# Kernel tuning notes

Measured on AMD Instinct MI355X. Metric: run time of the kernel, lower is better.

## Reference

```python
import jax, jax.numpy as jnp
import numpy as np

EPS = 1e-6

def _det3(m):
    return (m[..., 0, 0] * m[..., 1, 1] * m[..., 2, 2]
            + m[..., 0, 1] * m[..., 1, 2] * m[..., 2, 0]
            + m[..., 1, 0] * m[..., 2, 1] * m[..., 0, 2]
            - m[..., 2, 0] * m[..., 1, 1] * m[..., 0, 2]
            - m[..., 0, 0] * m[..., 2, 1] * m[..., 1, 2]
            - m[..., 1, 0] * m[..., 0, 1] * m[..., 2, 2])

def _inv3(m):
    a, b, c = m[..., 0, 0], m[..., 0, 1], m[..., 0, 2]
    d, e, f = m[..., 1, 0], m[..., 1, 1], m[..., 1, 2]
    g, h, i = m[..., 2, 0], m[..., 2, 1], m[..., 2, 2]
    adj = jnp.stack([
        jnp.stack([e * i - f * h, c * h - b * i, b * f - c * e], -1),
        jnp.stack([f * g - d * i, a * i - c * g, c * d - a * f], -1),
        jnp.stack([d * h - e * g, b * g - a * h, a * e - b * d], -1)], -2)
    return adj / _det3(m)[..., None, None]

def setup_inputs() -> dict:
    key = jax.random.key(0)
    ks = jax.random.split(key, 12)
    N, B, DH = 100000, 2048, 256
    idx = jnp.sort(jnp.concatenate([jnp.arange(B, dtype=jnp.int32),
                                    jax.random.randint(ks[0], (N - B,), 0, B, dtype=jnp.int32)]))
    return {
        "t": jax.random.uniform(ks[1], (B, 1), jnp.float32, 0.01, 0.99),
        "h": jax.random.normal(ks[2], (N, DH), jnp.float32),
        "pos": jax.random.normal(ks[3], (N, 3), jnp.float32),
        "eps_h": jax.random.normal(ks[4], (N, DH), jnp.float32),
        "eps_pos": jax.random.normal(ks[5], (N, 3), jnp.float32),
        "gparam_h": jax.random.normal(ks[6], (1, 1), jnp.float32),
        "gparam_pos": jax.random.normal(ks[7], (1, 1), jnp.float32),
        "W_mu": jax.random.normal(ks[8], (DH, DH), jnp.float32) / np.sqrt(DH),
        "W_r1": jax.random.normal(ks[9], (DH, 2 * DH), jnp.float32) / np.sqrt(DH),
        "W_r2": jax.random.normal(ks[10], (2 * DH, DH), jnp.float32) / np.sqrt(2 * DH),
        "index": idx,
        "num_graphs": B,
    }


def _forward(t, h, pos, eps_h, eps_pos, gparam_h, gparam_pos, W_mu, W_r1, W_r2, index, B):
    eye = jnp.eye(3, dtype=h.dtype)
    seg_sum = lambda x: jax.ops.segment_sum(x, index, num_segments=B)
    counts = seg_sum(jnp.ones((index.shape[0],), h.dtype))  # [B]

    def scatter_center(x):  # x - per-graph mean, gathered back
        mean = seg_sum(x) / counts[:, None]
        return x - mean[index]

    # volatility g(t): per-graph, gathered to nodes
    g_h = (0.1 + jax.nn.softplus(gparam_h) * t)[index]      # [N,1]
    g_pos = (0.1 + jax.nn.softplus(gparam_pos) * t)[index]  # [N,1]

    def f_net(t_, hh, pp):  # surrogate forward transformation f
        tn = t_[index]                                      # [N,1]
        mu_h = (hh @ W_mu) * (1.0 - tn)
        sigma_h = 0.1 + 0.9 * tn                            # [N,1]
        mu_pos = pp * (1.0 - tn)
        nrm = pp / (jnp.linalg.norm(pp, axis=-1, keepdims=True) + EPS)
        a = (0.2 + 0.8 * tn)[..., None]                     # [N,1,1]
        b = (0.1 * tn)[..., None]
        U = a * eye + b * (nrm[:, :, None] * nrm[:, None, :])  # [N,3,3]
        return mu_h, sigma_h, mu_pos, U

    def z_pos_fn(mu, U, eps):
        return mu + scatter_center(jnp.einsum('nij,nj->ni', U, eps))

    def score_pos_fn(eps, U, inv_U=None, C=None):
        if inv_U is None or C is None:
            inv_U = _inv3(U)
            inv_V = _inv3(seg_sum(inv_U))
            C = inv_V[index] @ (inv_U - eye)
        y = jnp.einsum('nji,nj->ni', inv_U, eps)
        ybar = seg_sum(y)
        c = jnp.einsum('nji,nj->ni', C, ybar[index])
        return scatter_center(c - y)  # zero_cog_score=True

    def solve_pos_fn(U, prel):
        inv_U = _inv3(U)
        inv_V = _inv3(seg_sum(inv_U))
        C = inv_V[index] @ (inv_U - eye)
        c = seg_sum(jnp.einsum('nij,nj->ni', C, prel))[index]
        eps = jnp.einsum('nij,nj->ni', inv_U, prel - c)
        return eps, inv_U, C

    bdrift = lambda dz, score, g: dz - 0.5 * g ** 2 * score

    # ---- target backward drift (time_derivative via jvp over t) ----
    (mu_h, sig_h, mu_p, U), (dmu_h, dsig_h, dmu_p, dU) = jax.jvp(
        lambda tt: f_net(tt, h, pos), (t,), (jnp.ones_like(t),))
    z_h = mu_h + sig_h * eps_h
    dz_h = dmu_h + dsig_h * eps_h
    z_p = z_pos_fn(mu_p, U, eps_pos)
    dz_p = z_pos_fn(dmu_p, dU, eps_pos)
    tgt_h = bdrift(dz_h, -eps_h / sig_h, g_h)
    tgt_p = bdrift(dz_p, score_pos_fn(eps_pos, U), g_pos)

    # ---- approximate backward drift ('x0' parameterization) ----
    h_r = jnp.tanh(z_h @ W_r1) @ W_r2   # reconstructor r
    pos_r = z_p * 0.9
    (mu_h2, sig_h2, mu_p2, U2), (dmu_h2, dsig_h2, dmu_p2, dU2) = jax.jvp(
        lambda tt: f_net(tt, h_r, pos_r), (t,), (jnp.ones_like(t),))
    eps_h2 = (z_h - mu_h2) / sig_h2
    eps_p2, inv_U2, C2 = solve_pos_fn(U2, z_p - mu_p2)
    dz_h2 = dmu_h2 + dsig_h2 * eps_h2
    dz_p2 = z_pos_fn(dmu_p2, dU2, eps_p2)
    apx_h = bdrift(dz_h2, -eps_h2 / sig_h2, g_h)
    apx_p = bdrift(dz_p2, score_pos_fn(eps_p2, U2, inv_U2, C2), g_pos)

    # ---- 'simple' loss: mse(approx/g, target/g) ----
    loss_h = jnp.mean(((apx_h - tgt_h) / g_h) ** 2)
    loss_p = jnp.mean(((apx_p - tgt_p) / g_pos) ** 2)
    return loss_h, loss_p


def reference(t, h, pos, eps_h, eps_pos, gparam_h, gparam_pos, W_mu, W_r1, W_r2, index, num_graphs):
    return _forward(t, h, pos, eps_h, eps_pos, gparam_h, gparam_pos, W_mu, W_r1, W_r2, index, num_graphs)
```

## Files before the change

kernel.cpp:

```cpp
#include <hip/hip_runtime.h>
#include <math.h>

#define NTHREADS 256
#define EPSC 1e-6f
#define NPL 3

typedef short bf16x8 __attribute__((ext_vector_type(8)));
typedef float f32x4  __attribute__((ext_vector_type(4)));

#define GLDS(srcp, dstp) __builtin_amdgcn_global_load_lds( \
    (const __attribute__((address_space(1))) void*)(srcp), \
    (__attribute__((address_space(3))) void*)(dstp), 16, 0, 0)

__device__ __forceinline__ ushort f2bf(float x) {
  union { float f; unsigned u; } v; v.f = x;
  unsigned r = v.u + 0x7FFFu + ((v.u >> 16) & 1u);
  return (ushort)(r >> 16);
}
__device__ __forceinline__ float bf2f(ushort x) {
  union { unsigned u; float f; } v; v.u = ((unsigned)x) << 16;
  return v.f;
}
__device__ __forceinline__ float tanh_fast(float x) {
  float xc = fminf(fmaxf(x, -15.f), 15.f);
  float e = __expf(2.f * xc);
  return (e - 1.f) / (e + 1.f);
}

__device__ __forceinline__ void inv3x3(const float m[9], float o[9]) {
  float a=m[0],b=m[1],c=m[2],d=m[3],e=m[4],f=m[5],g=m[6],h=m[7],i=m[8];
  float det = a*e*i + b*f*g + d*h*c - g*e*c - a*h*f - d*b*i;
  float r = 1.0f/det;
  o[0]=(e*i-f*h)*r; o[1]=(c*h-b*i)*r; o[2]=(b*f-c*e)*r;
  o[3]=(f*g-d*i)*r; o[4]=(a*i-c*g)*r; o[5]=(c*d-a*f)*r;
  o[6]=(d*h-e*g)*r; o[7]=(b*g-a*h)*r; o[8]=(a*e-b*d)*r;
}

__device__ __forceinline__ float wred(float v) {
#pragma unroll
  for (int o = 32; o > 0; o >>= 1) v += __shfl_xor(v, o, 64);
  return v;
}

__global__ __launch_bounds__(64) void pos_fused(
    int N, const float* __restrict__ pos, const float* __restrict__ epsp,
    const int* __restrict__ index, const float* __restrict__ t,
    const float* __restrict__ gpp, double* __restrict__ lossp)
{
  const int b = blockIdx.x;
  const int lane = threadIdx.x;

  int lo = 0, hi = N;
  while (lo < hi) { int mid = (lo + hi) >> 1; if (index[mid] < b) lo = mid + 1; else hi = mid; }
  const int start = lo;
  hi = N;
  while (lo < hi) { int mid = (lo + hi) >> 1; if (index[mid] < b + 1) lo = mid + 1; else hi = mid; }
  const int end = lo;
  const int cnt = end - start;
  const float fn = (float)cnt, rc = 1.0f / fn;

  const float tn  = t[b];
  const float a1  = 0.2f + 0.8f*tn, b1 = 0.1f*tn;
  const float omt = 1.0f - tn;
  const float sp  = log1pf(expf(gpp[0]));
  const float gp  = 0.1f + sp*tn;
  const float hg  = 0.5f*gp*gp;
  const float rgp = 1.0f/gp;
  const float pscale = 1.0f - 0.9f*omt;

  float iU[NPL][9], yv[NPL][3], wv[NPL][3], dwv[NPL][3], pv[NPL][3];
  float Vs[9] = {0}, wb[3] = {0}, dwb[3] = {0}, yb[3] = {0};
#pragma unroll
  for (int k = 0; k < NPL; ++k) {
    const int n = start + k*64 + lane;
    if (n < end) {
      const float px = pos[3*(size_t)n+0], py = pos[3*(size_t)n+1], pz = pos[3*(size_t)n+2];
      const float ex = epsp[3*(size_t)n+0], ey = epsp[3*(size_t)n+1], ez = epsp[3*(size_t)n+2];
      pv[k][0]=px; pv[k][1]=py; pv[k][2]=pz;
      const float pn = sqrtf(px*px+py*py+pz*pz) + EPSC;
      const float nx = px/pn, ny = py/pn, nz = pz/pn;
      const float nd = nx*ex + ny*ey + nz*ez;
      wv[k][0]=a1*ex + b1*nd*nx; wv[k][1]=a1*ey + b1*nd*ny; wv[k][2]=a1*ez + b1*nd*nz;
      dwv[k][0]=0.8f*ex + 0.1f*nd*nx; dwv[k][1]=0.8f*ey + 0.1f*nd*ny; dwv[k][2]=0.8f*ez + 0.1f*nd*nz;
      const float U[9] = { a1 + b1*nx*nx, b1*nx*ny,      b1*nx*nz,
                           b1*ny*nx,      a1 + b1*ny*ny, b1*ny*nz,
                           b1*nz*nx,      b1*nz*ny,      a1 + b1*nz*nz };
      inv3x3(U, iU[k]);
      yv[k][0] = iU[k][0]*ex + iU[k][3]*ey + iU[k][6]*ez;
      yv[k][1] = iU[k][1]*ex + iU[k][4]*ey + iU[k][7]*ez;
      yv[k][2] = iU[k][2]*ex + iU[k][5]*ey + iU[k][8]*ez;
#pragma unroll
      for (int j = 0; j < 9; ++j) Vs[j] += iU[k][j];
#pragma unroll
      for (int j = 0; j < 3; ++j) { wb[j]+=wv[k][j]; dwb[j]+=dwv[k][j]; yb[j]+=yv[k][j]; }
    }
  }
#pragma unroll
  for (int j = 0; j < 9; ++j) Vs[j] = wred(Vs[j]);
#pragma unroll
  for (int j = 0; j < 3; ++j) { wb[j]=wred(wb[j]); dwb[j]=wred(dwb[j]); yb[j]=wred(yb[j]); }

  float iV[9]; inv3x3(Vs, iV);
  float wm[3], dwm[3], u1[3], s1m[3];
#pragma unroll
  for (int i = 0; i < 3; ++i) { wm[i] = wb[i]*rc; dwm[i] = dwb[i]*rc; }
#pragma unroll
  for (int i = 0; i < 3; ++i) u1[i] = iV[0*3+i]*yb[0] + iV[1*3+i]*yb[1] + iV[2*3+i]*yb[2];
#pragma unroll
  for (int i = 0; i < 3; ++i) {
    const float csy = Vs[0*3+i]*u1[0] + Vs[1*3+i]*u1[1] + Vs[2*3+i]*u1[2] - fn*u1[i];
    s1m[i] = (csy - yb[i]) * rc;
  }

  float tg[NPL][3], zp[NPL][3], iU2[NPL][9], qv[NPL][3];
  float Vs2[9] = {0}, qs[3] = {0}, ps[3] = {0};
#pragma unroll
  for (int k = 0; k < NPL; ++k) {
    const int n = start + k*64 + lane;
    if (n < end) {
#pragma unroll
      for (int i = 0; i < 3; ++i) {
        const float c1 = iU[k][0*3+i]*u1[0] + iU[k][1*3+i]*u1[1] + iU[k][2*3+i]*u1[2] - u1[i];
        const float score1 = c1 - yv[k][i] - s1m[i];
        tg[k][i] = -pv[k][i] + dwv[k][i] - dwm[i] - hg*score1;
        zp[k][i] = pv[k][i]*omt + wv[k][i] - wm[i];
      }
      const float rx = 0.9f*zp[k][0], ry = 0.9f*zp[k][1], rz = 0.9f*zp[k][2];
      const float rn = sqrtf(rx*rx+ry*ry+rz*rz) + EPSC;
      const float nx = rx/rn, ny = ry/rn, nz = rz/rn;
      const float U2[9] = { a1 + b1*nx*nx, b1*nx*ny,      b1*nx*nz,
                            b1*ny*nx,      a1 + b1*ny*ny, b1*ny*nz,
                            b1*nz*nx,      b1*nz*ny,      a1 + b1*nz*nz };
      inv3x3(U2, iU2[k]);
      float prel[3];
#pragma unroll
      for (int i = 0; i < 3; ++i) prel[i] = zp[k][i]*pscale;
#pragma unroll
      for (int i = 0; i < 3; ++i)
        qv[k][i] = iU2[k][i*3+0]*prel[0] + iU2[k][i*3+1]*prel[1] + iU2[k][i*3+2]*prel[2];
#pragma unroll
      for (int j = 0; j < 9; ++j) Vs2[j] += iU2[k][j];
#pragma unroll
      for (int j = 0; j < 3; ++j) { qs[j] += qv[k][j]; ps[j] += prel[j]; }
    }
  }
#pragma unroll
  for (int j = 0; j < 9; ++j) Vs2[j] = wred(Vs2[j]);
#pragma unroll
  for (int j = 0; j < 3; ++j) { qs[j] = wred(qs[j]); ps[j] = wred(ps[j]); }

  float iV2[9]; inv3x3(Vs2, iV2);
  float cb2[3];
#pragma unroll
  for (int i = 0; i < 3; ++i)
    cb2[i] = iV2[i*3+0]*(qs[0]-ps[0]) + iV2[i*3+1]*(qs[1]-ps[1]) + iV2[i*3+2]*(qs[2]-ps[2]);

  float y2v[NPL][3], dw2v[NPL][3];
  float yb2[3] = {0}, dwb2[3] = {0};
#pragma unroll
  for (int k = 0; k < NPL; ++k) {
    const int n = start + k*64 + lane;
    if (n < end) {
      float e[3];
#pragma unroll
      for (int i = 0; i < 3; ++i)
        e[i] = qv[k][i] - (iU2[k][i*3+0]*cb2[0] + iU2[k][i*3+1]*cb2[1] + iU2[k][i*3+2]*cb2[2]);
#pragma unroll
      for (int i = 0; i < 3; ++i)
        y2v[k][i] = iU2[k][0*3+i]*e[0] + iU2[k][1*3+i]*e[1] + iU2[k][2*3+i]*e[2];
      const float rx = 0.9f*zp[k][0], ry = 0.9f*zp[k][1], rz = 0.9f*zp[k][2];
      const float rn = sqrtf(rx*rx+ry*ry+rz*rz) + EPSC;
      const float nx = rx/rn, ny = ry/rn, nz = rz/rn;
      const float nd = nx*e[0] + ny*e[1] + nz*e[2];
      dw2v[k][0] = 0.8f*e[0] + 0.1f*nd*nx;
      dw2v[k][1] = 0.8f*e[1] + 0.1f*nd*ny;
      dw2v[k][2] = 0.8f*e[2] + 0.1f*nd*nz;
#pragma unroll
      for (int j = 0; j < 3; ++j) { yb2[j] += y2v[k][j]; dwb2[j] += dw2v[k][j]; }
    }
  }
#pragma unroll
  for (int j = 0; j < 3; ++j) { yb2[j] = wred(yb2[j]); dwb2[j] = wred(dwb2[j]); }

  float u2[3], s2m[3], dw2m[3];
#pragma unroll
  for (int i = 0; i < 3; ++i) u2[i] = iV2[0*3+i]*yb2[0] + iV2[1*3+i]*yb2[1] + iV2[2*3+i]*yb2[2];
#pragma unroll
  for (int i = 0; i < 3; ++i) {
    const float csy = Vs2[0*3+i]*u2[0] + Vs2[1*3+i]*u2[1] + Vs2[2*3+i]*u2[2] - fn*u2[i];
    s2m[i] = (csy - yb2[i]) * rc;
    dw2m[i] = dwb2[i] * rc;
  }

  float acc = 0.0f;
#pragma unroll
  for (int k = 0; k < NPL; ++k) {
    const int n = start + k*64 + lane;
    if (n < end) {
#pragma unroll
      for (int i = 0; i < 3; ++i) {
        const float c2 = iU2[k][0*3+i]*u2[0] + iU2[k][1*3+i]*u2[1] + iU2[k][2*3+i]*u2[2] - u2[i];
        const float score2 = c2 - y2v[k][i] - s2m[i];
        const float dz2 = -0.9f*zp[k][i] + dw2v[k][i] - dw2m[i];
        const float apx = dz2 - hg*score2;
        const float d = (apx - tg[k][i]) * rgp;
        acc += d*d;
      }
    }
  }
  acc = wred(acc);
  if (lane == 0) atomicAdd(lossp, (double)acc);
}

__global__ __launch_bounds__(NTHREADS) void cvt_bf16(
    const float4* __restrict__ in, ushort4* __restrict__ out, int n4)
{
  for (int i = blockIdx.x*blockDim.x + threadIdx.x; i < n4; i += gridDim.x*blockDim.x) {
    float4 v = in[i];
    out[i] = make_ushort4(f2bf(v.x), f2bf(v.y), f2bf(v.z), f2bf(v.w));
  }
}

__global__ __launch_bounds__(NTHREADS) void transpose_cvt(
    const float* __restrict__ in, ushort* __restrict__ out, int K, int Nn)
{
  __shared__ float ts[32][33];
  const int tx = threadIdx.x & 31, ty = threadIdx.x >> 5;
  const int nb = blockIdx.x*32, kb = blockIdx.y*32;
#pragma unroll
  for (int r = 0; r < 4; ++r)
    ts[ty + r*8][tx] = in[(size_t)(kb + ty + r*8)*Nn + nb + tx];
  __syncthreads();
#pragma unroll
  for (int r = 0; r < 4; ++r)
    out[(size_t)(nb + ty + r*8)*K + kb + tx] = f2bf(ts[tx][ty + r*8]);
}

__global__ __launch_bounds__(256) void gemm_wcomb(
    const ushort* __restrict__ A, const ushort* __restrict__ Bt,
    int K, int Nn, int Mvalid, ushort* __restrict__ OutB)
{
  __shared__ __align__(16) ushort As[128*32];
  __shared__ __align__(16) ushort Bs[128*32];
  const int tid = threadIdx.x;
  const int row0 = blockIdx.y*128, col0 = blockIdx.x*128;
  const int wave = tid >> 6, lane = tid & 63;
  const int wm = (wave & 1)*64, wn = (wave >> 1)*64;
  const int lm = lane & 15, lq = lane >> 4;

  f32x4 acc[4][4];
#pragma unroll
  for (int i = 0; i < 4; ++i)
#pragma unroll
    for (int j = 0; j < 4; ++j) { acc[i][j][0]=0.f; acc[i][j][1]=0.f; acc[i][j][2]=0.f; acc[i][j][3]=0.f; }

  const int c0 = tid, c1 = tid + 256;
  const int r0a = c0 >> 2, k0a = (c0 & 3) << 3;
  const int r1a = c1 >> 2, k1a = (c1 & 3) << 3;

  for (int k0 = 0; k0 < K; k0 += 32) {
    __syncthreads();
    GLDS(A  + (size_t)(row0 + r0a)*K + k0 + k0a, As + c0*8);
    GLDS(A  + (size_t)(row0 + r1a)*K + k0 + k1a, As + c1*8);
    GLDS(Bt + (size_t)(col0 + r0a)*K + k0 + k0a, Bs + c0*8);
    GLDS(Bt + (size_t)(col0 + r1a)*K + k0 + k1a, Bs + c1*8);
    __syncthreads();

    bf16x8 af[4], bfr[4];
#pragma unroll
    for (int i = 0; i < 4; ++i)
      af[i] = *(const bf16x8*)&As[(wm + i*16 + lm)*32 + lq*8];
#pragma unroll
    for (int j = 0; j < 4; ++j)
      bfr[j] = *(const bf16x8*)&Bs[(wn + j*16 + lm)*32 + lq*8];
#pragma unroll
    for (int i = 0; i < 4; ++i)
#pragma unroll
      for (int j = 0; j < 4; ++j)
        acc[i][j] = __builtin_amdgcn_mfma_f32_16x16x32_bf16(af[i], bfr[j], acc[i][j], 0, 0, 0);
  }

#pragma unroll
  for (int i = 0; i < 4; ++i) {
#pragma unroll
    for (int reg = 0; reg < 4; ++reg) {
      const int r = row0 + wm + i*16 + lq*4 + reg;
#pragma unroll
      for (int j = 0; j < 4; ++j) {
        const int cc = col0 + wn + j*16 + lm;
        OutB[(size_t)cc*Mvalid + r] = f2bf(acc[i][j][reg]);
      }
    }
  }
}

__global__ __launch_bounds__(256, 2) void fused_h(
    const ushort* __restrict__ hb, const ushort* __restrict__ wmut,
    const ushort* __restrict__ wr1t, const ushort* __restrict__ wct,
    const float* __restrict__ eps, const int* __restrict__ index,
    const float* __restrict__ t, const float* __restrict__ gph,
    int N, double* __restrict__ lossAcc)
{
  __shared__ __align__(16) ushort zs[64*256];
  __shared__ __align__(16) ushort t1s[64*128];
  __shared__ __align__(16) ushort bstg[4*4096];

  const int tid = threadIdx.x;
  const int row0 = blockIdx.x * 64;
  const int wave = tid >> 6, lane = tid & 63;
  const int lm = lane & 15, lq = lane >> 4;
  const int wn  = wave * 64;
  const int wn2 = wave * 32;
  ushort* const bsw = bstg + wave*4096;

  bf16x8 af[8][4];
#pragma unroll
  for (int k = 0; k < 4; ++k)
#pragma unroll
    for (int i = 0; i < 4; ++i)
      af[k][i] = *(const bf16x8*)(hb + (size_t)(row0 + i*16 + lm)*256 + k*32 + lq*8);

#pragma unroll
  for (int c = 0; c < 4; ++c) {
    const int ch = c*64 + lane;
    GLDS(wmut + (size_t)(wn + (ch>>2))*256 + ((ch&3)<<3), bsw + ch*8);
  }

  f32x4 acc1[4][4];
#pragma unroll
  for (int i = 0; i < 4; ++i)
#pragma unroll
    for (int j = 0; j < 4; ++j) { acc1[i][j][0]=0.f; acc1[i][j][1]=0.f; acc1[i][j][2]=0.f; acc1[i][j][3]=0.f; }

#pragma unroll
  for (int k = 0; k < 8; ++k) {
    if (k < 4) {
#pragma unroll
      for (int i = 0; i < 4; ++i)
        af[k+4][i] = *(const bf16x8*)(hb + (size_t)(row0 + i*16 + lm)*256 + (k+4)*32 + lq*8);
    }
    if (k < 7) {
#pragma unroll
      for (int c = 0; c < 4; ++c) {
        const int ch = c*64 + lane;
        GLDS(wmut + (size_t)(wn + (ch>>2))*256 + (k+1)*32 + ((ch&3)<<3),
             bsw + ((k+1)&1)*2048 + ch*8);
      }
    }
    if (k < 4)      { asm volatile("s_waitcnt vmcnt(8)" ::: "memory"); }
    else if (k < 7) { asm volatile("s_waitcnt vmcnt(4)" ::: "memory"); }
    else            { asm volatile("s_waitcnt vmcnt(0)" ::: "memory"); }
    __builtin_amdgcn_sched_barrier(0);

    const ushort* cb = bsw + (k&1)*2048;
    bf16x8 bfr[4];
#pragma unroll
    for (int j = 0; j < 4; ++j)
      bfr[j] = *(const bf16x8*)&cb[(j*16 + lm)*32 + lq*8];
#pragma unroll
    for (int i = 0; i < 4; ++i)
#pragma unroll
      for (int j = 0; j < 4; ++j)
        acc1[i][j] = __builtin_amdgcn_mfma_f32_16x16x32_bf16(af[k][i], bfr[j], acc1[i][j], 0, 0, 0);
  }

#pragma unroll
  for (int c = 0; c < 2; ++c) {
    const int ch = c*64 + lane;
    GLDS(wr1t + (size_t)(wn2 + (ch>>2))*256 + ((ch&3)<<3), bsw + ch*8);
  }

  unsigned hmp[4][4][2];
#pragma unroll
  for (int i = 0; i < 4; ++i) {
#pragma unroll
    for (int reg = 0; reg < 4; ++reg) {
      const int rb = i*16 + lq*4 + reg;
      const int r = row0 + rb;
      const int rcl = (r < N) ? r : (N - 1);
      const float tn = t[index[rcl]];
      const float s0 = 1.0f - tn, s1 = 0.1f + 0.9f*tn;
#pragma unroll
      for (int j = 0; j < 4; ++j) {
        const int cc = wn + j*16 + lm;
        const float hm = acc1[i][j][reg];
        const unsigned hv = (unsigned)f2bf(hm);
        if (reg & 1) hmp[i][j][reg >> 1] |= hv << 16;
        else         hmp[i][j][reg >> 1]  = hv;
        const float z = hm*s0 + s1*eps[(size_t)rcl*256 + cc];
        zs[rb*256 + (cc ^ ((rb & 7) << 3))] = f2bf(z);
      }
    }
  }
  __syncthreads();

  f32x4 accL[4][4];
#pragma unroll
  for (int i = 0; i < 4; ++i)
#pragma unroll
    for (int j = 0; j < 4; ++j) { accL[i][j][0]=0.f; accL[i][j][1]=0.f; accL[i][j][2]=0.f; accL[i][j][3]=0.f; }

  for (int c2 = 0; c2 < 4; ++c2) {
    f32x4 acct[4][2];
#pragma unroll
    for (int i = 0; i < 4; ++i)
#pragma unroll
      for (int j = 0; j < 2; ++j) { acct[i][j][0]=0.f; acct[i][j][1]=0.f; acct[i][j][2]=0.f; acct[i][j][3]=0.f; }

#pragma unroll
    for (int k = 0; k < 8; ++k) {
      if (k < 7) {
#pragma unroll
        for (int c = 0; c < 2; ++c) {
          const int ch = c*64 + lane;
          GLDS(wr1t + (size_t)(c2*128 + wn2 + (ch>>2))*256 + (k+1)*32 + ((ch&3)<<3),
               bsw + ((k+1)&1)*2048 + ch*8);
        }
        asm volatile("s_waitcnt vmcnt(2)" ::: "memory");
      } else {
        asm volatile("s_waitcnt vmcnt(0)" ::: "memory");
      }
      __builtin_amdgcn_sched_barrier(0);

      const ushort* cb = bsw + (k&1)*2048;
      bf16x8 azf[4], bfr[2];
#pragma unroll
      for (int i = 0; i < 4; ++i) {
        const int r = i*16 + lm;
        const int c = k*32 + lq*8;
        azf[i] = *(const bf16x8*)&zs[r*256 + (c ^ ((r & 7) << 3))];
      }
#pragma unroll
      for (int j = 0; j < 2; ++j)
        bfr[j] = *(const bf16x8*)&cb[(j*16 + lm)*32 + lq*8];
#pragma unroll
      for (int i = 0; i < 4; ++i)
#pragma unroll
        for (int j = 0; j < 2; ++j)
          acct[i][j] = __builtin_amdgcn_mfma_f32_16x16x32_bf16(azf[i], bfr[j], acct[i][j], 0, 0, 0);
    }

#pragma unroll
    for (int c = 0; c < 4; ++c) {
      const int ch = c*64 + lane;
      GLDS(wct + (size_t)(wn + (ch>>2))*512 + c2*128 + ((ch&3)<<3), bsw + ch*8);
    }
    __syncthreads();

#pragma unroll
    for (int i = 0; i < 4; ++i)
#pragma unroll
      for (int j = 0; j < 2; ++j)
#pragma unroll
        for (int reg = 0; reg < 4; ++reg) {
          const int rb = i*16 + lq*4 + reg;
          const int c = wn2 + j*16 + lm;
          t1s[rb*128 + (c ^ ((rb & 7) << 3))] = f2bf(tanh_fast(acct[i][j][reg]));
        }
    __syncthreads();

#pragma unroll
    for (int k = 0; k < 4; ++k) {
      if (k < 3) {
#pragma unroll
        for (int c = 0; c < 4; ++c) {
          const int ch = c*64 + lane;
          GLDS(wct + (size_t)(wn + (ch>>2))*512 + c2*128 + (k+1)*32 + ((ch&3)<<3),
               bsw + ((k+1)&1)*2048 + ch*8);
        }
        asm volatile("s_waitcnt vmcnt(4)" ::: "memory");
      } else {
        asm volatile("s_waitcnt vmcnt(0)" ::: "memory");
      }
      __builtin_amdgcn_sched_barrier(0);

      const ushort* cb = bsw + (k&1)*2048;
      bf16x8 atf[4], bfr[4];
#pragma unroll
      for (int i = 0; i < 4; ++i) {
        const int r = i*16 + lm;
        const int c = k*32 + lq*8;
        atf[i] = *(const bf16x8*)&t1s[r*128 + (c ^ ((r & 7) << 3))];
      }
#pragma unroll
      for (int j = 0; j < 4; ++j)
        bfr[j] = *(const bf16x8*)&cb[(j*16 + lm)*32 + lq*8];
#pragma unroll
      for (int i = 0; i < 4; ++i)
#pragma unroll
        for (int j = 0; j < 4; ++j)
          accL[i][j] = __builtin_amdgcn_mfma_f32_16x16x32_bf16(atf[i], bfr[j], accL[i][j], 0, 0, 0);
    }

    if (c2 < 3) {
#pragma unroll
      for (int c = 0; c < 2; ++c) {
        const int ch = c*64 + lane;
        GLDS(wr1t + (size_t)((c2+1)*128 + wn2 + (ch>>2))*256 + ((ch&3)<<3), bsw + ch*8);
      }
    }
  }

  const float sp = log1pf(expf(gph[0]));
  float local = 0.f;
#pragma unroll
  for (int i = 0; i < 4; ++i) {
#pragma unroll
    for (int reg = 0; reg < 4; ++reg) {
      const int rb = i*16 + lq*4 + reg;
      const int r = row0 + rb;
      if (r < N) {
        const float tn = t[index[r]];
        const float gh  = 0.1f + sp*tn;
        const float sig = 0.1f + 0.9f*tn;
        const float fac = 1.0f + (0.9f + 0.5f*gh*gh/sig)*(1.0f - tn)/sig;
        const float sc  = fac/gh;
#pragma unroll
        for (int j = 0; j < 4; ++j) {
          const unsigned pw = hmp[i][j][reg >> 1];
          const ushort hv = (reg & 1) ? (ushort)(pw >> 16) : (ushort)(pw & 0xffffu);
          const float d = (bf2f(hv) - accL[i][j][reg]) * sc;
          local += d*d;
        }
      }
    }
  }
  double dv = (double)local;
#pragma unroll
  for (int off = 32; off > 0; off >>= 1) dv += __shfl_down(dv, off, 64);
  if (lane == 0) atomicAdd(lossAcc, dv);
}

__global__ void finalize_kernel(const double* lossh, const double* lossp,
                                float* out, int N, int DH)
{
  if (threadIdx.x == 0) {
    out[0] = (float)(lossh[0] / ((double)N * (double)DH));
    out[1] = (float)(lossp[0] / ((double)N * 3.0));
  }
}

extern "C" void kernel_launch(void* const* d_in, const int* in_sizes, int n_in,
                              void* d_out, int out_size, void* d_ws, size_t ws_size,
                              hipStream_t stream) {
  const float* t      = (const float*)d_in[0];
  const float* h      = (const float*)d_in[1];
  const float* pos    = (const float*)d_in[2];
  const float* eps_h  = (const float*)d_in[3];
  const float* eps_p  = (const float*)d_in[4];
  const float* gph    = (const float*)d_in[5];
  const float* gpp    = (const float*)d_in[6];
  const float* W_mu   = (const float*)d_in[7];
  const float* W_r1   = (const float*)d_in[8];
  const float* W_r2   = (const float*)d_in[9];
  const int*   index  = (const int*)d_in[10];
  const int B = in_sizes[0];
  const int N = in_sizes[10];
  const int DH = 256, DH2 = 512;
  const int NPAD = 100352;

  char* ws = (char*)d_ws;
  size_t off = 0;
  auto alloc = [&](size_t nbytes) { size_t o = off; off += (nbytes + 255) & ~(size_t)255; return o; };

  size_t o_loss = alloc(16);
  size_t o_hb   = alloc((size_t)NPAD*DH*2);
  size_t o_wmut = alloc((size_t)DH*DH*2);
  size_t o_wr1t = alloc((size_t)DH2*DH*2);
  size_t o_wr2b = alloc((size_t)DH2*DH*2);
  size_t o_wct  = alloc((size_t)DH*DH2*2);

  hipMemsetAsync(ws + o_loss, 0, 16, stream);

  double* lossh = (double*)(ws + o_loss);
  double* lossp = lossh + 1;
  ushort* hb   = (ushort*)(ws + o_hb);
  ushort* wmut = (ushort*)(ws + o_wmut);
  ushort* wr1t = (ushort*)(ws + o_wr1t);
  ushort* wr2b = (ushort*)(ws + o_wr2b);
  ushort* wct  = (ushort*)(ws + o_wct);

  pos_fused<<<B, 64, 0, stream>>>(N, pos, eps_p, index, t, gpp, lossp);

  cvt_bf16<<<2048, NTHREADS, 0, stream>>>((const float4*)h, (ushort4*)hb, N*DH/4);
  cvt_bf16<<<128, NTHREADS, 0, stream>>>((const float4*)W_r2, (ushort4*)wr2b, DH2*DH/4);
  transpose_cvt<<<dim3(DH/32,  DH/32), NTHREADS, 0, stream>>>(W_mu, wmut, DH, DH);
  transpose_cvt<<<dim3(DH2/32, DH/32), NTHREADS, 0, stream>>>(W_r1, wr1t, DH, DH2);

  gemm_wcomb<<<dim3(DH/128, DH2/128), 256, 0, stream>>>(
      wr2b, wmut, DH, DH, DH2, wct);

  const int mg64 = (N + 63) / 64;
  fused_h<<<mg64, 256, 0, stream>>>(
      hb, wmut, wr1t, wct, eps_h, index, t, gph, N, lossh);

  finalize_kernel<<<1, 64, 0, stream>>>(lossh, lossp, (float*)d_out, N, DH);
}
```

Before: 478.9 us.

## Merge prep kernels, fold pos path into main kernel, drop LDS weight staging

Combines the four conversion/transpose kernels into one multi-role launch and runs the per-graph position loss as extra blocks of the main h kernel, cutting the number of launches. The main kernel now reads weight fragments straight from global memory instead of staging them in LDS with async loads, which frees shared memory so launch bounds can rise to 3 blocks per CU. The combined weight matrix is stored negated so the second GEMM accumulates onto the first GEMM's accumulator, removing the packed hm registers and the subtraction. The risks are uncoalesced, higher-latency direct global weight loads with no explicit prefetch, and the pos blocks now sharing the grid with the GEMM blocks.

Result: slower. 545.5 us (+13.9%).

```diff
diff --git a/kernel.cpp b/kernel.cpp
--- a/kernel.cpp
+++ b/kernel.cpp
@@ -42,14 +42,12 @@
   return v;
 }
 
-__global__ __launch_bounds__(64) void pos_fused(
-    int N, const float* __restrict__ pos, const float* __restrict__ epsp,
+__device__ void pos_graph(
+    int b, int lane, int N,
+    const float* __restrict__ pos, const float* __restrict__ epsp,
     const int* __restrict__ index, const float* __restrict__ t,
     const float* __restrict__ gpp, double* __restrict__ lossp)
 {
-  const int b = blockIdx.x;
-  const int lane = threadIdx.x;
-
   int lo = 0, hi = N;
   while (lo < hi) { int mid = (lo + hi) >> 1; if (index[mid] < b) lo = mid + 1; else hi = mid; }
   const int start = lo;
@@ -212,28 +210,47 @@
   if (lane == 0) atomicAdd(lossp, (double)acc);
 }
 
-__global__ __launch_bounds__(NTHREADS) void cvt_bf16(
-    const float4* __restrict__ in, ushort4* __restrict__ out, int n4)
-{
-  for (int i = blockIdx.x*blockDim.x + threadIdx.x; i < n4; i += gridDim.x*blockDim.x) {
-    float4 v = in[i];
-    out[i] = make_ushort4(f2bf(v.x), f2bf(v.y), f2bf(v.z), f2bf(v.w));
-  }
-}
-
-__global__ __launch_bounds__(NTHREADS) void transpose_cvt(
-    const float* __restrict__ in, ushort* __restrict__ out, int K, int Nn)
+__global__ __launch_bounds__(NTHREADS) void prep_all(
+    const float4* __restrict__ h, ushort4* __restrict__ hb, int n4h,
+    const float4* __restrict__ wr2, ushort4* __restrict__ wr2b, int n4w,
+    const float* __restrict__ wmu, ushort* __restrict__ wmut,
+    const float* __restrict__ wr1, ushort* __restrict__ wr1t)
 {
   __shared__ float ts[32][33];
-  const int tx = threadIdx.x & 31, ty = threadIdx.x >> 5;
-  const int nb = blockIdx.x*32, kb = blockIdx.y*32;
-#pragma unroll
-  for (int r = 0; r < 4; ++r)
-    ts[ty + r*8][tx] = in[(size_t)(kb + ty + r*8)*Nn + nb + tx];
-  __syncthreads();
-#pragma unroll
-  for (int r = 0; r < 4; ++r)
-    out[(size_t)(nb + ty + r*8)*K + kb + tx] = f2bf(ts[tx][ty + r*8]);
+  const int bid = blockIdx.x;
+  if (bid < 2048) {
+    for (int i = bid*NTHREADS + threadIdx.x; i < n4h; i += 2048*NTHREADS) {
+      float4 v = h[i];
+      hb[i] = make_ushort4(f2bf(v.x), f2bf(v.y), f2bf(v.z), f2bf(v.w));
+    }
+  } else if (bid < 2176) {
+    for (int i = (bid-2048)*NTHREADS + threadIdx.x; i < n4w; i += 128*NTHREADS) {
+      float4 v = wr2[i];
+      wr2b[i] = make_ushort4(f2bf(v.x), f2bf(v.y), f2bf(v.z), f2bf(v.w));
+    }
+  } else if (bid < 2240) {
+    const int vb = bid - 2176;
+    const int nb = (vb & 7)*32, kb = (vb >> 3)*32;
+    const int tx = threadIdx.x & 31, ty = threadIdx.x >> 5;
+#pragma unroll
+    for (int r = 0; r < 4; ++r)
+      ts[ty + r*8][tx] = wmu[(size_t)(kb + ty + r*8)*256 + nb + tx];
+    __syncthreads();
+#pragma unroll
+    for (int r = 0; r < 4; ++r)
+      wmut[(size_t)(nb + ty + r*8)*256 + kb + tx] = f2bf(ts[tx][ty + r*8]);
+  } else {
+    const int vb = bid - 2240;
+    const int nb = (vb & 15)*32, kb = (vb >> 4)*32;
+    const int tx = threadIdx.x & 31, ty = threadIdx.x >> 5;
+#pragma unroll
+    for (int r = 0; r < 4; ++r)
+      ts[ty + r*8][tx] = wr1[(size_t)(kb + ty + r*8)*512 + nb + tx];
+    __syncthreads();
+#pragma unroll
+    for (int r = 0; r < 4; ++r)
+      wr1t[(size_t)(nb + ty + r*8)*256 + kb + tx] = f2bf(ts[tx][ty + r*8]);
+  }
 }
 
 __global__ __launch_bounds__(256) void gemm_wcomb(
@@ -288,13 +305,16 @@
 #pragma unroll
       for (int j = 0; j < 4; ++j) {
         const int cc = col0 + wn + j*16 + lm;
-        OutB[(size_t)cc*Mvalid + r] = f2bf(acc[i][j][reg]);
-      }
-    }
-  }
-}
-
-__global__ __launch_bounds__(256, 2) void fused_h(
+        OutB[(size_t)cc*Mvalid + r] = f2bf(-acc[i][j][reg]);
+      }
+    }
+  }
+}
+
+__global__ __launch_bounds__(256, 3) void fused_main(
+    int PB, int Bg,
+    const float* __restrict__ pos, const float* __restrict__ epsp,
+    const float* __restrict__ gpp, double* __restrict__ lossp,
     const ushort* __restrict__ hb, const ushort* __restrict__ wmut,
     const ushort* __restrict__ wr1t, const ushort* __restrict__ wct,
     const float* __restrict__ eps, const int* __restrict__ index,
@@ -303,74 +323,42 @@
 {
   __shared__ __align__(16) ushort zs[64*256];
   __shared__ __align__(16) ushort t1s[64*128];
-  __shared__ __align__(16) ushort bstg[4*4096];
-
-  const int tid = threadIdx.x;
-  const int row0 = blockIdx.x * 64;
-  const int wave = tid >> 6, lane = tid & 63;
+
+  const int wave = threadIdx.x >> 6, lane = threadIdx.x & 63;
+
+  if (blockIdx.x < PB) {
+    const int b = blockIdx.x*4 + wave;
+    if (b < Bg) pos_graph(b, lane, N, pos, epsp, index, t, gpp, lossp);
+    return;
+  }
+
+  const int row0 = (blockIdx.x - PB) * 64;
   const int lm = lane & 15, lq = lane >> 4;
   const int wn  = wave * 64;
   const int wn2 = wave * 32;
-  ushort* const bsw = bstg + wave*4096;
-
-  bf16x8 af[8][4];
-#pragma unroll
-  for (int k = 0; k < 4; ++k)
+
+  f32x4 acc[4][4];
+#pragma unroll
+  for (int i = 0; i < 4; ++i)
+#pragma unroll
+    for (int j = 0; j < 4; ++j) { acc[i][j][0]=0.f; acc[i][j][1]=0.f; acc[i][j][2]=0.f; acc[i][j][3]=0.f; }
+
+#pragma unroll
+  for (int k = 0; k < 8; ++k) {
+    bf16x8 a_[4], b_[4];
 #pragma unroll
     for (int i = 0; i < 4; ++i)
-      af[k][i] = *(const bf16x8*)(hb + (size_t)(row0 + i*16 + lm)*256 + k*32 + lq*8);
-
-#pragma unroll
-  for (int c = 0; c < 4; ++c) {
-    const int ch = c*64 + lane;
-    GLDS(wmut + (size_t)(wn + (ch>>2))*256 + ((ch&3)<<3), bsw + ch*8);
-  }
-
-  f32x4 acc1[4][4];
-#pragma unroll
-  for (int i = 0; i < 4; ++i)
-#pragma unroll
-    for (int j = 0; j < 4; ++j) { acc1[i][j][0]=0.f; acc1[i][j][1]=0.f; acc1[i][j][2]=0.f; acc1[i][j][3]=0.f; }
-
-#pragma unroll
-  for (int k = 0; k < 8; ++k) {
-    if (k < 4) {
-#pragma unroll
-      for (int i = 0; i < 4; ++i)
-        af[k+4][i] = *(const bf16x8*)(hb + (size_t)(row0 + i*16 + lm)*256 + (k+4)*32 + lq*8);
-    }
-    if (k < 7) {
-#pragma unroll
-      for (int c = 0; c < 4; ++c) {
-        const int ch = c*64 + lane;
-        GLDS(wmut + (size_t)(wn + (ch>>2))*256 + (k+1)*32 + ((ch&3)<<3),
-             bsw + ((k+1)&1)*2048 + ch*8);
-      }
-    }
-    if (k < 4)      { asm volatile("s_waitcnt vmcnt(8)" ::: "memory"); }
-    else if (k < 7) { asm volatile("s_waitcnt vmcnt(4)" ::: "memory"); }
-    else            { asm volatile("s_waitcnt vmcnt(0)" ::: "memory"); }
-    __builtin_amdgcn_sched_barrier(0);
-
-    const ushort* cb = bsw + (k&1)*2048;
-    bf16x8 bfr[4];
+      a_[i] = *(const bf16x8*)(hb + (size_t)(row0 + i*16 + lm)*256 + k*32 + lq*8);
 #pragma unroll
     for (int j = 0; j < 4; ++j)
-      bfr[j] = *(const bf16x8*)&cb[(j*16 + lm)*32 + lq*8];
+      b_[j] = *(const bf16x8*)(wmut + (size_t)(wn + j*16 + lm)*256 + k*32 + lq*8);
 #pragma unroll
     for (int i = 0; i < 4; ++i)
 #pragma unroll
       for (int j = 0; j < 4; ++j)
-        acc1[i][j] = __builtin_amdgcn_mfma_f32_16x16x32_bf16(af[k][i], bfr[j], acc1[i][j], 0, 0, 0);
-  }
-
-#pragma unroll
-  for (int c = 0; c < 2; ++c) {
-    const int ch = c*64 + lane;
-    GLDS(wr1t + (size_t)(wn2 + (ch>>2))*256 + ((ch&3)<<3), bsw + ch*8);
-  }
-
-  unsigned hmp[4][4][2];
+        acc[i][j] = __builtin_amdgcn_mfma_f32_16x16x32_bf16(a_[i], b_[j], acc[i][j], 0, 0, 0);
+  }
+
 #pragma unroll
   for (int i = 0; i < 4; ++i) {
 #pragma unroll
@@ -383,22 +371,12 @@
 #pragma unroll
       for (int j = 0; j < 4; ++j) {
         const int cc = wn + j*16 + lm;
-        const float hm = acc1[i][j][reg];
-        const unsigned hv = (unsigned)f2bf(hm);
-        if (reg & 1) hmp[i][j][reg >> 1] |= hv << 16;
-        else         hmp[i][j][reg >> 1]  = hv;
-        const float z = hm*s0 + s1*eps[(size_t)rcl*256 + cc];
+        const float z = acc[i][j][reg]*s0 + s1*eps[(size_t)rcl*256 + cc];
         zs[rb*256 + (cc ^ ((rb & 7) << 3))] = f2bf(z);
       }
     }
   }
   __syncthreads();
-
-  f32x4 accL[4][4];
-#pragma unroll
-  for (int i = 0; i < 4; ++i)
-#pragma unroll
-    for (int j = 0; j < 4; ++j) { accL[i][j][0]=0.f; accL[i][j][1]=0.f; accL[i][j][2]=0.f; accL[i][j][3]=0.f; }
 
   for (int c2 = 0; c2 < 4; ++c2) {
     f32x4 acct[4][2];
@@ -409,44 +387,29 @@
 
 #pragma unroll
     for (int k = 0; k < 8; ++k) {
-      if (k < 7) {
-#pragma unroll
-        for (int c = 0; c < 2; ++c) {
-          const int ch = c*64 + lane;
-          GLDS(wr1t + (size_t)(c2*128 + wn2 + (ch>>2))*256 + (k+1)*32 + ((ch&3)<<3),
-               bsw + ((k+1)&1)*2048 + ch*8);
-        }
-        asm volatile("s_waitcnt vmcnt(2)" ::: "memory");
-      } else {
-        asm volatile("s_waitcnt vmcnt(0)" ::: "memory");
-      }
-      __builtin_amdgcn_sched_barrier(0);
-
-      const ushort* cb = bsw + (k&1)*2048;
-      bf16x8 azf[4], bfr[2];
+      bf16x8 az[4], b_[2];
 #pragma unroll
       for (int i = 0; i < 4; ++i) {
         const int r = i*16 + lm;
         const int c = k*32 + lq*8;
-        azf[i] = *(const bf16x8*)&zs[r*256 + (c ^ ((r & 7) << 3))];
+        az[i] = *(const bf16x8*)&zs[r*256 + (c ^ ((r & 7) << 3))];
       }
 #pragma unroll
       for (int j = 0; j < 2; ++j)
-        bfr[j] = *(const bf16x8*)&cb[(j*16 + lm)*32 + lq*8];
+        b_[j] = *(const bf16x8*)(wr1t + (size_t)(c2*128 + wn2 + j*16 + lm)*256 + k*32 + lq*8);
 #pragma unroll
       for (int i = 0; i < 4; ++i)
 #pragma unroll
         for (int j = 0; j < 2; ++j)
-          acct[i][j] = __builtin_amdgcn_mfma_f32_16x16x32_bf16(azf[i], bfr[j], acct[i][j], 0, 0, 0);
-    }
-
-#pragma unroll
-    for (int c = 0; c < 4; ++c) {
-      const int ch = c*64 + lane;
-      GLDS(wct + (size_t)(wn + (ch>>2))*512 + c2*128 + ((ch&3)<<3), bsw + ch*8);
-    }
+          acct[i][j] = __builtin_amdgcn_mfma_f32_16x16x32_bf16(az[i], b_[j], acct[i][j], 0, 0, 0);
+    }
+
+    bf16x8 pb[4];
+#pragma unroll
+    for (int j = 0; j < 4; ++j)
+      pb[j] = *(const bf16x8*)(wct + (size_t)(wn + j*16 + lm)*512 + c2*128 + lq*8);
+
     __syncthreads();
-
 #pragma unroll
     for (int i = 0; i < 4; ++i)
 #pragma unroll
@@ -461,43 +424,26 @@
 
 #pragma unroll
     for (int k = 0; k < 4; ++k) {
-      if (k < 3) {
-#pragma unroll
-        for (int c = 0; c < 4; ++c) {
-          const int ch = c*64 + lane;
-          GLDS(wct + (size_t)(wn + (ch>>2))*512 + c2*128 + (k+1)*32 + ((ch&3)<<3),
-               bsw + ((k+1)&1)*2048 + ch*8);
-        }
-        asm volatile("s_waitcnt vmcnt(4)" ::: "memory");
-      } else {
-        asm volatile("s_waitcnt vmcnt(0)" ::: "memory");
-      }
-      __builtin_amdgcn_sched_barrier(0);
-
-      const ushort* cb = bsw + (k&1)*2048;
-      bf16x8 atf[4], bfr[4];
+      bf16x8 at[4], b_[4];
 #pragma unroll
       for (int i = 0; i < 4; ++i) {
         const int r = i*16 + lm;
         const int c = k*32 + lq*8;
-        atf[i] = *(const bf16x8*)&t1s[r*128 + (c ^ ((r & 7) << 3))];
-      }
-#pragma unroll
-      for (int j = 0; j < 4; ++j)
-        bfr[j] = *(const bf16x8*)&cb[(j*16 + lm)*32 + lq*8];
+        at[i] = *(const bf16x8*)&t1s[r*128 + (c ^ ((r & 7) << 3))];
+      }
+      if (k == 0) {
+#pragma unroll
+        for (int j = 0; j < 4; ++j) b_[j] = pb[j];
+      } else {
+#pragma unroll
+        for (int j = 0; j < 4; ++j)
+          b_[j] = *(const bf16x8*)(wct + (size_t)(wn + j*16 + lm)*512 + c2*128 + k*32 + lq*8);
+      }
 #pragma unroll
       for (int i = 0; i < 4; ++i)
 #pragma unroll
         for (int j = 0; j < 4; ++j)
-          accL[i][j] = __builtin_amdgcn_mfma_f32_16x16x32_bf16(atf[i], bfr[j], accL[i][j], 0, 0, 0);
-    }
-
-    if (c2 < 3) {
-#pragma unroll
-      for (int c = 0; c < 2; ++c) {
-        const int ch = c*64 + lane;
-        GLDS(wr1t + (size_t)((c2+1)*128 + wn2 + (ch>>2))*256 + ((ch&3)<<3), bsw + ch*8);
-      }
+          acc[i][j] = __builtin_amdgcn_mfma_f32_16x16x32_bf16(at[i], b_[j], acc[i][j], 0, 0, 0);
     }
   }
 
@@ -507,8 +453,7 @@
   for (int i = 0; i < 4; ++i) {
 #pragma unroll
     for (int reg = 0; reg < 4; ++reg) {
-      const int rb = i*16 + lq*4 + reg;
-      const int r = row0 + rb;
+      const int r = row0 + i*16 + lq*4 + reg;
       if (r < N) {
         const float tn = t[index[r]];
         const float gh  = 0.1f + sp*tn;
@@ -517,9 +462,7 @@
         const float sc  = fac/gh;
 #pragma unroll
         for (int j = 0; j < 4; ++j) {
-          const unsigned pw = hmp[i][j][reg >> 1];
-          const ushort hv = (reg & 1) ? (ushort)(pw >> 16) : (ushort)(pw & 0xffffu);
-          const float d = (bf2f(hv) - accL[i][j][reg]) * sc;
+          const float d = acc[i][j][reg] * sc;
           local += d*d;
         }
       }
@@ -580,18 +523,18 @@
   ushort* wr2b = (ushort*)(ws + o_wr2b);
   ushort* wct  = (ushort*)(ws + o_wct);
 
-  pos_fused<<<B, 64, 0, stream>>>(N, pos, eps_p, index, t, gpp, lossp);
-
-  cvt_bf16<<<2048, NTHREADS, 0, stream>>>((const float4*)h, (ushort4*)hb, N*DH/4);
-  cvt_bf16<<<128, NTHREADS, 0, stream>>>((const float4*)W_r2, (ushort4*)wr2b, DH2*DH/4);
-  transpose_cvt<<<dim3(DH/32,  DH/32), NTHREADS, 0, stream>>>(W_mu, wmut, DH, DH);
-  transpose_cvt<<<dim3(DH2/32, DH/32), NTHREADS, 0, stream>>>(W_r1, wr1t, DH, DH2);
+  prep_all<<<2368, NTHREADS, 0, stream>>>(
+      (const float4*)h, (ushort4*)hb, N*DH/4,
+      (const float4*)W_r2, (ushort4*)wr2b, DH2*DH/4,
+      W_mu, wmut, W_r1, wr1t);
 
   gemm_wcomb<<<dim3(DH/128, DH2/128), 256, 0, stream>>>(
       wr2b, wmut, DH, DH, DH2, wct);
 
-  const int mg64 = (N + 63) / 64;
-  fused_h<<<mg64, 256, 0, stream>>>(
+  const int PB = (B + 3) / 4;
+  const int HB = (N + 63) / 64;
+  fused_main<<<PB + HB, 256, 0, stream>>>(
+      PB, B, pos, eps_p, gpp, lossp,
       hb, wmut, wr1t, wct, eps_h, index, t, gph, N, lossh);
 
   finalize_kernel<<<1, 64, 0, stream>>>(lossh, lossp, (float*)d_out, N, DH);
```
